# Kernel optimization log

Measured on AMD Instinct MI355X. Metric: run time of the kernel, lower is better.

## Reference

```python
import jax, jax.numpy as jnp
import numpy as np

B, T, F, H, NQ = 256, 512, 128, 256, 4


def setup_inputs() -> dict:
    key = jax.random.key(0)
    ks = jax.random.split(key, 7)
    s = 0.1
    return {
        "x": jax.random.normal(ks[0], (B, T, F), dtype=jnp.float32),
        "W_in": jax.random.normal(ks[1], (F + H, NQ), dtype=jnp.float32) * s,
        "b_in": jax.random.normal(ks[2], (NQ,), dtype=jnp.float32) * s,
        "Wq": jax.random.normal(ks[3], (4, NQ, NQ), dtype=jnp.float32) * s,
        "bq": jax.random.normal(ks[4], (4, NQ), dtype=jnp.float32) * s,
        "W_out": jax.random.normal(ks[5], (NQ, H), dtype=jnp.float32) * s,
        "b_out": jax.random.normal(ks[6], (H,), dtype=jnp.float32) * s,
    }


def reference(x, W_in, b_in, Wq, bq, W_out, b_out):
    # x: [B, T, F] (batch_first). Sequential LSTM-like recurrence via lax.scan.
    batch = x.shape[0]
    hidden = W_out.shape[1]

    def step(carry, x_t):
        h, c = carry
        v = jnp.concatenate([h, x_t], axis=1)              # [B, H+F]
        y = v @ W_in + b_in                                # [B, NQ]
        # 4 VQC branches (classical surrogate: tanh(linear)), vectorized over k
        q = jnp.tanh(jnp.einsum('bq,kqr->kbr', y, Wq) + bq[:, None, :])  # [4, B, NQ]
        z = jnp.einsum('kbq,qh->kbh', q, W_out) + b_out    # [4, B, H]
        i = jax.nn.sigmoid(z[0])
        f = jax.nn.sigmoid(z[1])
        g = jnp.tanh(z[2])
        o = jax.nn.sigmoid(z[3])
        c = f * c + i * g
        h = o * jnp.tanh(c)
        return (h, c), h

    h0 = jnp.zeros((batch, hidden), dtype=x.dtype)
    c0 = jnp.zeros((batch, hidden), dtype=x.dtype)
    (h_T, c_T), hs = jax.lax.scan(step, (h0, c0), jnp.swapaxes(x, 0, 1))
    hidden_seq = jnp.swapaxes(hs, 0, 1)                    # [B, T, H]
    return hidden_seq, (h_T, c_T)
```

## Files before the change

### kernel.cpp

```cpp
#include <hip/hip_runtime.h>


#define B_ 256
#define T_ 512
#define F_ 128
#define H_ 256

#define SC1 1.442695041f
#define SC2 2.885390082f
#define ISC2 0.3465735903f

__device__ __forceinline__ float rcp_f(float x)  { return __builtin_amdgcn_rcpf(x); }
__device__ __forceinline__ float exp2_f(float x) { return __builtin_amdgcn_exp2f(x); }

__device__ __forceinline__ float rl(float v, int lane) {
    return __int_as_float(__builtin_amdgcn_readlane(__float_as_int(v), lane));
}

__device__ __forceinline__ void tree4(float& p0, float& p1, float& p2, float& p3) {
    asm volatile(
        "s_nop 1\n\t"
        "v_add_f32_dpp %0, %0, %0 quad_perm:[1,0,3,2] row_mask:0xf bank_mask:0xf\n\t"
        "v_add_f32_dpp %1, %1, %1 quad_perm:[1,0,3,2] row_mask:0xf bank_mask:0xf\n\t"
        "v_add_f32_dpp %2, %2, %2 quad_perm:[1,0,3,2] row_mask:0xf bank_mask:0xf\n\t"
        "v_add_f32_dpp %3, %3, %3 quad_perm:[1,0,3,2] row_mask:0xf bank_mask:0xf\n\t"
        "v_add_f32_dpp %0, %0, %0 quad_perm:[2,3,0,1] row_mask:0xf bank_mask:0xf\n\t"
        "v_add_f32_dpp %1, %1, %1 quad_perm:[2,3,0,1] row_mask:0xf bank_mask:0xf\n\t"
        "v_add_f32_dpp %2, %2, %2 quad_perm:[2,3,0,1] row_mask:0xf bank_mask:0xf\n\t"
        "v_add_f32_dpp %3, %3, %3 quad_perm:[2,3,0,1] row_mask:0xf bank_mask:0xf\n\t"
        "v_add_f32_dpp %0, %0, %0 row_half_mirror row_mask:0xf bank_mask:0xf\n\t"
        "v_add_f32_dpp %1, %1, %1 row_half_mirror row_mask:0xf bank_mask:0xf\n\t"
        "v_add_f32_dpp %2, %2, %2 row_half_mirror row_mask:0xf bank_mask:0xf\n\t"
        "v_add_f32_dpp %3, %3, %3 row_half_mirror row_mask:0xf bank_mask:0xf\n\t"
        "v_add_f32_dpp %0, %0, %0 row_mirror row_mask:0xf bank_mask:0xf\n\t"
        "v_add_f32_dpp %1, %1, %1 row_mirror row_mask:0xf bank_mask:0xf\n\t"
        "v_add_f32_dpp %2, %2, %2 row_mirror row_mask:0xf bank_mask:0xf\n\t"
        "v_add_f32_dpp %3, %3, %3 row_mirror row_mask:0xf bank_mask:0xf\n\t"
        "v_add_f32_dpp %0, %0, %0 row_bcast:15 row_mask:0xf bank_mask:0xf\n\t"
        "v_add_f32_dpp %1, %1, %1 row_bcast:15 row_mask:0xf bank_mask:0xf\n\t"
        "v_add_f32_dpp %2, %2, %2 row_bcast:15 row_mask:0xf bank_mask:0xf\n\t"
        "v_add_f32_dpp %3, %3, %3 row_bcast:15 row_mask:0xf bank_mask:0xf\n\t"
        "v_add_f32_dpp %0, %0, %0 row_bcast:31 row_mask:0xf bank_mask:0xf\n\t"
        "v_add_f32_dpp %1, %1, %1 row_bcast:31 row_mask:0xf bank_mask:0xf\n\t"
        "v_add_f32_dpp %2, %2, %2 row_bcast:31 row_mask:0xf bank_mask:0xf\n\t"
        "v_add_f32_dpp %3, %3, %3 row_bcast:31 row_mask:0xf bank_mask:0xf"
        : "+v"(p0), "+v"(p1), "+v"(p2), "+v"(p3));
}

__device__ __forceinline__ void lds_barrier() {
    asm volatile("s_waitcnt lgkmcnt(0)\n\ts_barrier" ::: "memory");
}

__global__ __launch_bounds__(256, 1) void qlstm_kernel(
    const float* __restrict__ x,
    const float* __restrict__ W_in,
    const float* __restrict__ b_in,
    const float* __restrict__ Wq,
    const float* __restrict__ bq,
    const float* __restrict__ W_out,
    const float* __restrict__ b_out,
    float* __restrict__ out)
{
    const int b = blockIdx.x;
    const int g = threadIdx.x;
    const int w = g >> 6;
    const int l = g & 63;

    __shared__ float partA[2][16][4];

    const float4* Win4 = (const float4*)W_in;

    float4 t4 = Win4[g];
    float wh[4] = {t4.x, t4.y, t4.z, t4.w};

    const bool has_x = (w < 2);
    float wx[4] = {0.f, 0.f, 0.f, 0.f};
    if (has_x) {
        float4 u4 = Win4[H_ + g];
        wx[0] = u4.x; wx[1] = u4.y; wx[2] = u4.z; wx[3] = u4.w;
    }

    const float sk[4] = {-SC1, -SC1, SC2, -SC1};
    float wo2[4][4];
    float bo2[4];
    {
        const float bo = b_out[g];
        float wos[4];
        float wsum = 0.f;
#pragma unroll
        for (int r = 0; r < 4; ++r) { wos[r] = W_out[r * H_ + g]; wsum += wos[r]; }
#pragma unroll
        for (int k = 0; k < 4; ++k) {
            bo2[k] = sk[k] * (bo + wsum);
#pragma unroll
            for (int r = 0; r < 4; ++r) wo2[k][r] = -2.0f * sk[k] * wos[r];
        }
    }

    float bin[4];
#pragma unroll
    for (int q = 0; q < 4; ++q) bin[q] = b_in[q];

    const int m = l & 15, qk = m >> 2, qr = m & 3;
    float wql[4];
#pragma unroll
    for (int s = 0; s < 4; ++s) wql[s] = Wq[qk * 16 + s * 4 + qr];
    float bql = bq[qk * 4 + qr];
#pragma unroll
    for (int s = 0; s < 4; ++s) bql = fmaf(bin[s], wql[s], bql);
    bql *= SC2;
#pragma unroll
    for (int s = 0; s < 4; ++s) wql[s] *= SC2;
    const float bqlw = (w == 0) ? bql : 0.0f;

    float tau = 0.f, C = 0.f;
    float owh0 = 0.f, owh1 = 0.f, owh2 = 0.f, owh3 = 0.f;

    const float* xp = x + (size_t)b * T_ * F_ + g;
    float xq0 = 0.f, xq1 = 0.f, xq2 = 0.f, xq3 = 0.f;
    float xv1 = 0.f;
    if (has_x) {
        const float xv0 = xp[0];
        xv1 = xp[F_];
        xq0 = xv0 * wx[0]; xq1 = xv0 * wx[1];
        xq2 = xv0 * wx[2]; xq3 = xv0 * wx[3];
    }

    float* outp = out + (size_t)b * T_ * H_ + g;
    float o_last = 0.f;

#define STEP(t, slot)                                                          \
    {                                                                          \
        float p0 = fmaf(tau, owh0, xq0);                                       \
        float p1 = fmaf(tau, owh1, xq1);                                       \
        float p2 = fmaf(tau, owh2, xq2);                                       \
        float p3 = fmaf(tau, owh3, xq3);                                       \
        tree4(p0, p1, p2, p3);                                                 \
                \
        float u = fmaf(p0, wql[0], bqlw);                                      \
        const float vv = fmaf(p3, wql[3], p2 * wql[2]);                        \
        u = fmaf(p1, wql[1], u);                                               \
        const float aqw = u + vv;                                              \
        if (l >= 48) partA[slot][m][w] = aqw;                                  \
        lds_barrier();                                                         \
        const float4 a = *(const float4*)&partA[slot][m][0];                   \
         \
        if (has_x) {                                                           \
            xq0 = xv1 * wx[0]; xq1 = xv1 * wx[1];                              \
            xq2 = xv1 * wx[2]; xq3 = xv1 * wx[3];                              \
            int tn = (t) + 2; if (tn >= T_) tn = T_ - 1;                       \
            xv1 = xp[(size_t)tn * F_];                                         \
        }                                                                      \
        const float aq = (a.x + a.y) + (a.z + a.w);                            \
        const float qp = rcp_f(1.0f + exp2_f(aq));     \
        float qs[16];                                                          \
        _Pragma("unroll")                                                      \
        for (int i = 0; i < 16; ++i) qs[i] = rl(qp, i);                        \
        float zp[4];                                                           \
        _Pragma("unroll")                                                      \
        for (int k = 0; k < 4; ++k) {                                          \
            float za = fmaf(qs[k * 4 + 0], wo2[k][0], bo2[k]);                 \
            const float zb = fmaf(qs[k * 4 + 1], wo2[k][1],                    \
                                  qs[k * 4 + 2] * wo2[k][2]);                  \
            za = fmaf(qs[k * 4 + 3], wo2[k][3], za);                           \
            zp[k] = za + zb;                                                   \
        }                                                                      \
        const float e0 = exp2_f(zp[0]);                                        \
        const float e1 = exp2_f(zp[1]);                                        \
        const float E2 = exp2_f(zp[2]);                                        \
        const float e3 = exp2_f(zp[3]);                                        \
        const float num2 = fmaf(SC2, E2, -SC2);                                \
        const float IG2  = num2 * rcp_f((1.0f + e0) * (1.0f + E2));            \
        const float fg   = rcp_f(1.0f + e1);                                   \
        C = fmaf(fg, C, IG2);                                                  \
                \
        const float o = rcp_f(1.0f + e3);                                      \
        owh0 = o * wh[0]; owh1 = o * wh[1];                                    \
        owh2 = o * wh[2]; owh3 = o * wh[3];                                    \
        const float Ec = exp2_f(C);                                            \
        tau = (Ec - 1.0f) * rcp_f(1.0f + Ec);                                  \
        o_last = o;                                                            \
        outp[(size_t)(t) * H_] = tau * o;                 \
    }

    for (int t = 0; t < T_; t += 2) {
        STEP(t, 0);
        STEP(t + 1, 1);
    }
#undef STEP

    float* hT = out + (size_t)B_ * T_ * H_;
    hT[(size_t)b * H_ + g] = tau * o_last;
    hT[(size_t)B_ * H_ + (size_t)b * H_ + g] = C * ISC2;
}

extern "C" void kernel_launch(void* const* d_in, const int* in_sizes, int n_in,
                              void* d_out, int out_size, void* d_ws, size_t ws_size,
                              hipStream_t stream) {
    const float* x     = (const float*)d_in[0];
    const float* W_in  = (const float*)d_in[1];
    const float* b_in  = (const float*)d_in[2];
    const float* Wq    = (const float*)d_in[3];
    const float* bq    = (const float*)d_in[4];
    const float* W_out = (const float*)d_in[5];
    const float* b_out = (const float*)d_in[6];
    float* out = (float*)d_out;

    qlstm_kernel<<<dim3(B_), dim3(256), 0, stream>>>(
        x, W_in, b_in, Wq, bq, W_out, b_out, out);
}
```

Measured before the change: 369.9 us.

## Replace per-step workgroup barrier with LDS flag-based spin synchronization

Each recurrence step used to synchronize the four wavefronts with s_barrier after publishing partial sums to LDS. Now each wave writes its partial and a step tag flag to LDS, then polls the flags with ds_read_b128 until all four tags match, reading data and flags together. The aim is to avoid the cost of the full barrier on the serial critical path. It relies on LDS write ordering within a wave so data is visible before the flag, and spinning may burn issue slots or race if ordering is not guaranteed.

```diff
diff --git a/kernel.cpp b/kernel.cpp
--- a/kernel.cpp
+++ b/kernel.cpp
@@ -10,12 +10,17 @@
 #define SC2 2.885390082f
 #define ISC2 0.3465735903f
 
+typedef float f4v __attribute__((ext_vector_type(4)));
+typedef int   i4v __attribute__((ext_vector_type(4)));
+
 __device__ __forceinline__ float rcp_f(float x)  { return __builtin_amdgcn_rcpf(x); }
 __device__ __forceinline__ float exp2_f(float x) { return __builtin_amdgcn_exp2f(x); }
 
 __device__ __forceinline__ float rl(float v, int lane) {
     return __int_as_float(__builtin_amdgcn_readlane(__float_as_int(v), lane));
 }
+
+__device__ __forceinline__ int imin2(int a, int b) { return a < b ? a : b; }
 
 __device__ __forceinline__ void tree4(float& p0, float& p1, float& p2, float& p3) {
     asm volatile(
@@ -47,10 +52,6 @@
         : "+v"(p0), "+v"(p1), "+v"(p2), "+v"(p3));
 }
 
-__device__ __forceinline__ void lds_barrier() {
-    asm volatile("s_waitcnt lgkmcnt(0)\n\ts_barrier" ::: "memory");
-}
-
 __global__ __launch_bounds__(256, 1) void qlstm_kernel(
     const float* __restrict__ x,
     const float* __restrict__ W_in,
@@ -66,7 +67,10 @@
     const int w = g >> 6;
     const int l = g & 63;
 
-    __shared__ float partA[2][16][4];
+    __shared__ __align__(16) float partA[2][16][4];
+    __shared__ __align__(16) int   flagsA[2][4];
+
+    if (g < 8) ((int*)flagsA)[g] = 0;
 
     const float4* Win4 = (const float4*)W_in;
 
@@ -112,6 +116,15 @@
 #pragma unroll
     for (int s = 0; s < 4; ++s) wql[s] *= SC2;
     const float bqlw = (w == 0) ? bql : 0.0f;
+
+    const unsigned daddr0 = (unsigned)(unsigned long long)&partA[0][m][0];
+    const unsigned daddr1 = (unsigned)(unsigned long long)&partA[1][m][0];
+    const unsigned faddr0 = (unsigned)(unsigned long long)&flagsA[0][0];
+    const unsigned faddr1 = (unsigned)(unsigned long long)&flagsA[1][0];
+    const unsigned waddr0 = (unsigned)(unsigned long long)&partA[0][m][w];
+    const unsigned waddr1 = (unsigned)(unsigned long long)&partA[1][m][w];
+    const unsigned fwadd0 = (unsigned)(unsigned long long)&flagsA[0][w];
+    const unsigned fwadd1 = (unsigned)(unsigned long long)&flagsA[1][w];
 
     float tau = 0.f, C = 0.f;
     float owh0 = 0.f, owh1 = 0.f, owh2 = 0.f, owh3 = 0.f;
@@ -129,8 +142,11 @@
     float* outp = out + (size_t)b * T_ * H_ + g;
     float o_last = 0.f;
 
-#define STEP(t, slot)                                                          \
+    __syncthreads();
+
+#define STEP(t_, slot_)                                                        \
     {                                                                          \
+        const int tag = (t_) + 1;                                              \
         float p0 = fmaf(tau, owh0, xq0);                                       \
         float p1 = fmaf(tau, owh1, xq1);                                       \
         float p2 = fmaf(tau, owh2, xq2);                                       \
@@ -141,15 +157,41 @@
         const float vv = fmaf(p3, wql[3], p2 * wql[2]);                        \
         u = fmaf(p1, wql[1], u);                                               \
         const float aqw = u + vv;                                              \
-        if (l >= 48) partA[slot][m][w] = aqw;                                  \
-        lds_barrier();                                                         \
-        const float4 a = *(const float4*)&partA[slot][m][0];                   \
-         \
+        if (l >= 48)                                                           \
+            asm volatile("ds_write_b32 %0, %1"                                 \
+                         :: "v"((slot_) ? waddr1 : waddr0), "v"(aqw)           \
+                         : "memory");                                          \
+        if (l == 63)                                                           \
+            asm volatile("ds_write_b32 %0, %1"                                 \
+                         :: "v"((slot_) ? fwadd1 : fwadd0), "v"(tag)           \
+                         : "memory");                                          \
+           \
+        i4v f; f4v a;                                                          \
+        asm volatile("ds_read_b128 %0, %2\n\t"                                 \
+                     "ds_read_b128 %1, %3"                                     \
+                     : "=&v"(f), "=&v"(a)                                      \
+                     : "v"((slot_) ? faddr1 : faddr0),                         \
+                       "v"((slot_) ? daddr1 : daddr0)                          \
+                     : "memory");                                              \
+           \
         if (has_x) {                                                           \
             xq0 = xv1 * wx[0]; xq1 = xv1 * wx[1];                              \
             xq2 = xv1 * wx[2]; xq3 = xv1 * wx[3];                              \
-            int tn = (t) + 2; if (tn >= T_) tn = T_ - 1;                       \
+            int tn = (t_) + 2; if (tn >= T_) tn = T_ - 1;                      \
             xv1 = xp[(size_t)tn * F_];                                         \
+        }                                                                      \
+        asm volatile("s_waitcnt lgkmcnt(0)" ::: "memory");                     \
+        __builtin_amdgcn_sched_barrier(0);                                     \
+           \
+        while (imin2(imin2(f.x, f.y), imin2(f.z, f.w)) != tag) {               \
+            asm volatile("ds_read_b128 %0, %2\n\t"                             \
+                         "ds_read_b128 %1, %3\n\t"                             \
+                         "s_waitcnt lgkmcnt(0)"                                \
+                         : "=&v"(f), "=&v"(a)                                  \
+                         : "v"((slot_) ? faddr1 : faddr0),                     \
+                           "v"((slot_) ? daddr1 : daddr0)                      \
+                         : "memory");                                          \
+            __builtin_amdgcn_sched_barrier(0);                                 \
         }                                                                      \
         const float aq = (a.x + a.y) + (a.z + a.w);                            \
         const float qp = rcp_f(1.0f + exp2_f(aq));     \
@@ -173,14 +215,14 @@
         const float IG2  = num2 * rcp_f((1.0f + e0) * (1.0f + E2));            \
         const float fg   = rcp_f(1.0f + e1);                                   \
         C = fmaf(fg, C, IG2);                                                  \
-                \
+                  \
         const float o = rcp_f(1.0f + e3);                                      \
         owh0 = o * wh[0]; owh1 = o * wh[1];                                    \
         owh2 = o * wh[2]; owh3 = o * wh[3];                                    \
         const float Ec = exp2_f(C);                                            \
         tau = (Ec - 1.0f) * rcp_f(1.0f + Ec);                                  \
         o_last = o;                                                            \
-        outp[(size_t)(t) * H_] = tau * o;                 \
+        outp[(size_t)(t_) * H_] = tau * o;                \
     }
 
     for (int t = 0; t < T_; t += 2) {
```

Result: no change. 373.6 us (+1.0%).
